# Kernel tuning notes

Measured on AMD Instinct MI355X. Metric: run time of the kernel, lower is better.

Reference implementation:

```python
import jax, jax.numpy as jnp
import numpy as np


def setup_inputs() -> dict:
    key = jax.random.key(0)
    k1, k2, k3 = jax.random.split(key, 3)
    B, S, D = 128, 1024, 64
    return {
        "q": jax.random.normal(k1, (B, S, D), dtype=jnp.float32),
        "k": jax.random.normal(k2, (B, S, D), dtype=jnp.float32),
        "v": jax.random.normal(k3, (B, S, D), dtype=jnp.float32),
    }


def reference(q, k, v):
    # Faithful to the torch module: NO 1/sqrt(d) scaling.
    # Chunking over batch dim in the original is math-equivalent to full bmm.
    scores = jnp.einsum("bsd,btd->bst", q, k)  # [B, S, S]
    attn = jax.nn.softmax(scores, axis=-1)
    return jnp.einsum("bst,btd->bsd", attn, v)  # [B, S, D]
```

## Files before the change

kernel.cpp:

```cpp
#include <hip/hip_runtime.h>
#include <math.h>

namespace {

typedef _Float16 half8 __attribute__((ext_vector_type(8)));
typedef float floatx4 __attribute__((ext_vector_type(4)));

constexpr int kS   = 1024;
constexpr int kD   = 64;
constexpr int kPad = 72;
constexpr float kLog2e = 1.4426950408889634f;
constexpr float kThr   = 8.0f;

union H4 { _Float16 h[4]; uint2 u2; };

__device__ __forceinline__ float fast_exp2(float x) {
#if __has_builtin(__builtin_amdgcn_exp2f)
  return __builtin_amdgcn_exp2f(x);
#else
  return exp2f(x);
#endif
}

__device__ __forceinline__ float fast_rcp(float x) {
#if __has_builtin(__builtin_amdgcn_rcpf)
  return __builtin_amdgcn_rcpf(x);
#else
  return 1.0f / x;
#endif
}

__device__ __forceinline__ unsigned pk2(float a, float b) {
#if __has_builtin(__builtin_amdgcn_cvt_pkrtz)
  auto h = __builtin_amdgcn_cvt_pkrtz(a, b);
  return __builtin_bit_cast(unsigned, h);
#else
  H4 t; t.h[0] = (_Float16)a; t.h[1] = (_Float16)b;
  return t.u2.x;
#endif
}

__global__ __launch_bounds__(256, 2)
void fa_mfma_kernel(const float* __restrict__ qg, const float* __restrict__ kg,
                    const float* __restrict__ vg, float* __restrict__ og) {
  __shared__ __align__(16) _Float16 sK [2][64][kPad];
  __shared__ __align__(16) _Float16 sVt[2][64][kPad];
  __shared__ __align__(16) _Float16 sP [256][kPad];

  const int tid  = threadIdx.x;
  const int lane = tid & 63;
  const int w    = __builtin_amdgcn_readfirstlane(tid >> 6);
  const int quad = lane >> 4;
  const int r    = lane & 15;

  const int blk = blockIdx.x;
  const int b     = (blk & 7) + 8 * (blk >> 5);
  const int qbase = ((blk >> 3) & 3) * 256;

  const float* qb = qg + (size_t)b * kS * kD;
  const float* kb = kg + (size_t)b * kS * kD;
  const float* vb = vg + (size_t)b * kS * kD;
  float*       ob = og + (size_t)b * kS * kD;

  half8 fqh[4][2], fql[4][2];
#pragma unroll
  for (int ntq = 0; ntq < 4; ++ntq)
#pragma unroll
    for (int ks = 0; ks < 2; ++ks) {
      const float* src =
          qb + (size_t)(qbase + w * 64 + ntq * 16 + r) * kD + ks * 32 + quad * 8;
      float4 a = ((const float4*)src)[0];
      float4 c = ((const float4*)src)[1];
      float f[8] = {a.x, a.y, a.z, a.w, c.x, c.y, c.z, c.w};
#pragma unroll
      for (int j = 0; j < 8; ++j) {
        float x = f[j] * kLog2e;
        _Float16 h = (_Float16)x;
        fqh[ntq][ks][j] = h;
        fql[ntq][ks][j] = (_Float16)(x - (float)h);
      }
    }

  float m_i[4] = {-INFINITY, -INFINITY, -INFINITY, -INFINITY};
  float l_i[4] = {0.f, 0.f, 0.f, 0.f};
  floatx4 O[4][4];
#pragma unroll
  for (int a = 0; a < 4; ++a)
#pragma unroll
    for (int c = 0; c < 4; ++c) O[a][c] = floatx4{0.f, 0.f, 0.f, 0.f};

  const int krow = tid >> 2, kc0 = (tid & 3) * 16;
  const int vkey4 = (tid & 15) * 4;
  const int vd0   = (tid >> 4) * 4;
  float4 kbuf[4], vbuf[4];

  auto load_kv = [&](int kt) {
    const float4* ksrc = (const float4*)(kb + (size_t)(kt * 64 + krow) * kD + kc0);
#pragma unroll
    for (int g = 0; g < 4; ++g) kbuf[g] = ksrc[g];
#pragma unroll
    for (int kk = 0; kk < 4; ++kk)
      vbuf[kk] = *(const float4*)(vb + (size_t)(kt * 64 + vkey4 + kk) * kD + vd0);
  };
  auto stage = [&](int bi) {
#pragma unroll
    for (int g = 0; g < 4; ++g) {
      float t[4] = {kbuf[g].x, kbuf[g].y, kbuf[g].z, kbuf[g].w};
      H4 hk;
#pragma unroll
      for (int j = 0; j < 4; ++j) hk.h[j] = (_Float16)t[j];
      *(uint2*)&sK[bi][krow][kc0 + g * 4] = hk.u2;
    }
    float tv[4][4];
#pragma unroll
    for (int kk = 0; kk < 4; ++kk) {
      tv[kk][0] = vbuf[kk].x; tv[kk][1] = vbuf[kk].y;
      tv[kk][2] = vbuf[kk].z; tv[kk][3] = vbuf[kk].w;
    }
#pragma unroll
    for (int j = 0; j < 4; ++j) {
      H4 hv;
#pragma unroll
      for (int kk = 0; kk < 4; ++kk) hv.h[kk] = (_Float16)tv[kk][j];
      *(uint2*)&sVt[bi][vd0 + j][vkey4] = hv.u2;
    }
  };

  auto softmax2 = [&](floatx4 (&S)[2][4], int base) {
    float pmax[2];
#pragma unroll
    for (int g = 0; g < 2; ++g) {
      float a0 = fmaxf(fmaxf(S[g][0][0], S[g][0][1]), fmaxf(S[g][0][2], S[g][0][3]));
      float a1 = fmaxf(fmaxf(S[g][1][0], S[g][1][1]), fmaxf(S[g][1][2], S[g][1][3]));
      float a2 = fmaxf(fmaxf(S[g][2][0], S[g][2][1]), fmaxf(S[g][2][2], S[g][2][3]));
      float a3 = fmaxf(fmaxf(S[g][3][0], S[g][3][1]), fmaxf(S[g][3][2], S[g][3][3]));
      pmax[g] = fmaxf(fmaxf(a0, a1), fmaxf(a2, a3));
    }
    const unsigned long long need =
        __ballot(pmax[0] > m_i[base] + kThr || pmax[1] > m_i[base + 1] + kThr);
    if (need) {
      float alpha[2];
#pragma unroll
      for (int g = 0; g < 2; ++g) {
        float t = pmax[g];
        t = fmaxf(t, __shfl_xor(t, 16, 64));
        t = fmaxf(t, __shfl_xor(t, 32, 64));
        const float mn = fmaxf(m_i[base + g], t);
        alpha[g] = fast_exp2(m_i[base + g] - mn);
        m_i[base + g] = mn;
        l_i[base + g] *= alpha[g];
      }
#pragma unroll
      for (int g = 0; g < 2; ++g)
#pragma unroll
        for (int j = 0; j < 4; ++j) {
          const float a = __shfl(alpha[g], quad * 4 + j, 64);
#pragma unroll
          for (int nd = 0; nd < 4; ++nd) O[base + g][nd][j] *= a;
        }
    }
#pragma unroll
    for (int g = 0; g < 2; ++g) {
      float rs = 0.f;
#pragma unroll
      for (int mt = 0; mt < 4; ++mt) {
        float p0 = fast_exp2(S[g][mt][0] - m_i[base + g]);
        float p1 = fast_exp2(S[g][mt][1] - m_i[base + g]);
        float p2 = fast_exp2(S[g][mt][2] - m_i[base + g]);
        float p3 = fast_exp2(S[g][mt][3] - m_i[base + g]);
        rs += (p0 + p1) + (p2 + p3);
        uint2 u; u.x = pk2(p0, p1); u.y = pk2(p2, p3);
        *(uint2*)&sP[w * 64 + (base + g) * 16 + r][mt * 16 + quad * 4] = u;
      }
      l_i[base + g] += rs;
    }
  };

  load_kv(0);
  stage(0);
  load_kv(1);

  for (int kt = 0; kt < kS / 64; ++kt) {
    const int cur = kt & 1, nxt = cur ^ 1;
    __syncthreads();
    stage(nxt);
    load_kv((kt + 2) & 15);

    floatx4 S0[2][4];
    __builtin_amdgcn_s_setprio(1);
#pragma unroll
    for (int mt = 0; mt < 4; ++mt) {
      half8 fk0 = *(const half8*)&sK[cur][mt * 16 + r][quad * 8];
      half8 fk1 = *(const half8*)&sK[cur][mt * 16 + r][32 + quad * 8];
#pragma unroll
      for (int g = 0; g < 2; ++g) {
        floatx4 s = {0.f, 0.f, 0.f, 0.f};
        s = __builtin_amdgcn_mfma_f32_16x16x32_f16(fk0, fqh[g][0], s, 0, 0, 0);
        s = __builtin_amdgcn_mfma_f32_16x16x32_f16(fk1, fqh[g][1], s, 0, 0, 0);
        s = __builtin_amdgcn_mfma_f32_16x16x32_f16(fk0, fql[g][0], s, 0, 0, 0);
        s = __builtin_amdgcn_mfma_f32_16x16x32_f16(fk1, fql[g][1], s, 0, 0, 0);
        S0[g][mt] = s;
      }
    }
    __builtin_amdgcn_s_setprio(0);

    softmax2(S0, 0);

    floatx4 S1[2][4];
    __builtin_amdgcn_s_setprio(1);
#pragma unroll
    for (int mt = 0; mt < 4; ++mt) {
      half8 fk0 = *(const half8*)&sK[cur][mt * 16 + r][quad * 8];
      half8 fk1 = *(const half8*)&sK[cur][mt * 16 + r][32 + quad * 8];
#pragma unroll
      for (int g = 0; g < 2; ++g) {
        floatx4 s = {0.f, 0.f, 0.f, 0.f};
        s = __builtin_amdgcn_mfma_f32_16x16x32_f16(fk0, fqh[2 + g][0], s, 0, 0, 0);
        s = __builtin_amdgcn_mfma_f32_16x16x32_f16(fk1, fqh[2 + g][1], s, 0, 0, 0);
        s = __builtin_amdgcn_mfma_f32_16x16x32_f16(fk0, fql[2 + g][0], s, 0, 0, 0);
        s = __builtin_amdgcn_mfma_f32_16x16x32_f16(fk1, fql[2 + g][1], s, 0, 0, 0);
        S1[g][mt] = s;
      }
    }
    __builtin_amdgcn_s_setprio(0);

    __builtin_amdgcn_s_setprio(1);
#pragma unroll
    for (int ks = 0; ks < 2; ++ks) {
      half8 fp0 = *(const half8*)&sP[w * 64 + 0 * 16 + r][ks * 32 + quad * 8];
      half8 fp1 = *(const half8*)&sP[w * 64 + 1 * 16 + r][ks * 32 + quad * 8];
#pragma unroll
      for (int nd = 0; nd < 4; ++nd) {
        half8 fv = *(const half8*)&sVt[cur][nd * 16 + r][ks * 32 + quad * 8];
        O[0][nd] = __builtin_amdgcn_mfma_f32_16x16x32_f16(fp0, fv, O[0][nd], 0, 0, 0);
        O[1][nd] = __builtin_amdgcn_mfma_f32_16x16x32_f16(fp1, fv, O[1][nd], 0, 0, 0);
      }
    }
    __builtin_amdgcn_s_setprio(0);

    softmax2(S1, 2);

    __builtin_amdgcn_s_setprio(1);
#pragma unroll
    for (int ks = 0; ks < 2; ++ks) {
      half8 fp2 = *(const half8*)&sP[w * 64 + 2 * 16 + r][ks * 32 + quad * 8];
      half8 fp3 = *(const half8*)&sP[w * 64 + 3 * 16 + r][ks * 32 + quad * 8];
#pragma unroll
      for (int nd = 0; nd < 4; ++nd) {
        half8 fv = *(const half8*)&sVt[cur][nd * 16 + r][ks * 32 + quad * 8];
        O[2][nd] = __builtin_amdgcn_mfma_f32_16x16x32_f16(fp2, fv, O[2][nd], 0, 0, 0);
        O[3][nd] = __builtin_amdgcn_mfma_f32_16x16x32_f16(fp3, fv, O[3][nd], 0, 0, 0);
      }
    }
    __builtin_amdgcn_s_setprio(0);
  }

#pragma unroll
  for (int mtq = 0; mtq < 4; ++mtq) {
    float t = l_i[mtq];
    t += __shfl_xor(t, 16, 64);
    t += __shfl_xor(t, 32, 64);
#pragma unroll
    for (int j = 0; j < 4; ++j) {
      const float lrow = __shfl(t, quad * 4 + j, 64);
      const float linv = fast_rcp(lrow);
      float* dst =
          ob + (size_t)(qbase + w * 64 + mtq * 16 + quad * 4 + j) * kD + r;
#pragma unroll
      for (int nd = 0; nd < 4; ++nd) dst[nd * 16] = O[mtq][nd][j] * linv;
    }
  }
}

}

extern "C" void kernel_launch(void* const* d_in, const int* in_sizes, int n_in,
                              void* d_out, int out_size, void* d_ws, size_t ws_size,
                              hipStream_t stream) {
  const float* q = (const float*)d_in[0];
  const float* k = (const float*)d_in[1];
  const float* v = (const float*)d_in[2];
  float* out = (float*)d_out;

  fa_mfma_kernel<<<dim3(512), 256, 0, stream>>>(q, k, v, out);
}
```

Baseline: 191.5 us.

## Load K fragments directly from global into registers, drop K LDS staging

K tiles are now read straight from global memory into per-lane MFMA fragments (converted to fp16 in registers) instead of being staged through shared memory. The next K tile is prefetched after the second softmax. The two PV MFMA blocks are merged into a single pass after both softmaxes. The row-max reduction now runs before the ballot, and the row-sum reduction runs every tile rather than once at the end. This removes LDS traffic and the K staging step, but adds redundant global reads of K (each wave loads the full tile), more registers, and extra shuffles on every tile.

```diff
diff --git a/kernel.cpp b/kernel.cpp
--- a/kernel.cpp
+++ b/kernel.cpp
@@ -30,20 +30,9 @@
 #endif
 }
 
-__device__ __forceinline__ unsigned pk2(float a, float b) {
-#if __has_builtin(__builtin_amdgcn_cvt_pkrtz)
-  auto h = __builtin_amdgcn_cvt_pkrtz(a, b);
-  return __builtin_bit_cast(unsigned, h);
-#else
-  H4 t; t.h[0] = (_Float16)a; t.h[1] = (_Float16)b;
-  return t.u2.x;
-#endif
-}
-
 __global__ __launch_bounds__(256, 2)
 void fa_mfma_kernel(const float* __restrict__ qg, const float* __restrict__ kg,
                     const float* __restrict__ vg, float* __restrict__ og) {
-  __shared__ __align__(16) _Float16 sK [2][64][kPad];
   __shared__ __align__(16) _Float16 sVt[2][64][kPad];
   __shared__ __align__(16) _Float16 sP [256][kPad];
 
@@ -89,28 +78,34 @@
 #pragma unroll
     for (int c = 0; c < 4; ++c) O[a][c] = floatx4{0.f, 0.f, 0.f, 0.f};
 
-  const int krow = tid >> 2, kc0 = (tid & 3) * 16;
+  half8 fk[4][2];
+  auto load_k = [&](int kt) {
+#pragma unroll
+    for (int mt = 0; mt < 4; ++mt)
+#pragma unroll
+      for (int ks = 0; ks < 2; ++ks) {
+        const float* s =
+            kb + (size_t)(kt * 64 + mt * 16 + r) * kD + ks * 32 + quad * 8;
+        float4 a = ((const float4*)s)[0];
+        float4 c = ((const float4*)s)[1];
+        half8 h;
+        h[0] = (_Float16)a.x; h[1] = (_Float16)a.y;
+        h[2] = (_Float16)a.z; h[3] = (_Float16)a.w;
+        h[4] = (_Float16)c.x; h[5] = (_Float16)c.y;
+        h[6] = (_Float16)c.z; h[7] = (_Float16)c.w;
+        fk[mt][ks] = h;
+      }
+  };
+
   const int vkey4 = (tid & 15) * 4;
   const int vd0   = (tid >> 4) * 4;
-  float4 kbuf[4], vbuf[4];
-
-  auto load_kv = [&](int kt) {
-    const float4* ksrc = (const float4*)(kb + (size_t)(kt * 64 + krow) * kD + kc0);
-#pragma unroll
-    for (int g = 0; g < 4; ++g) kbuf[g] = ksrc[g];
+  float4 vbuf[4];
+  auto load_v = [&](int kt) {
 #pragma unroll
     for (int kk = 0; kk < 4; ++kk)
       vbuf[kk] = *(const float4*)(vb + (size_t)(kt * 64 + vkey4 + kk) * kD + vd0);
   };
-  auto stage = [&](int bi) {
-#pragma unroll
-    for (int g = 0; g < 4; ++g) {
-      float t[4] = {kbuf[g].x, kbuf[g].y, kbuf[g].z, kbuf[g].w};
-      H4 hk;
-#pragma unroll
-      for (int j = 0; j < 4; ++j) hk.h[j] = (_Float16)t[j];
-      *(uint2*)&sK[bi][krow][kc0 + g * 4] = hk.u2;
-    }
+  auto stage_v = [&](int bi) {
     float tv[4][4];
 #pragma unroll
     for (int kk = 0; kk < 4; ++kk) {
@@ -127,25 +122,25 @@
   };
 
   auto softmax2 = [&](floatx4 (&S)[2][4], int base) {
-    float pmax[2];
+    float tm[2];
 #pragma unroll
     for (int g = 0; g < 2; ++g) {
       float a0 = fmaxf(fmaxf(S[g][0][0], S[g][0][1]), fmaxf(S[g][0][2], S[g][0][3]));
       float a1 = fmaxf(fmaxf(S[g][1][0], S[g][1][1]), fmaxf(S[g][1][2], S[g][1][3]));
       float a2 = fmaxf(fmaxf(S[g][2][0], S[g][2][1]), fmaxf(S[g][2][2], S[g][2][3]));
       float a3 = fmaxf(fmaxf(S[g][3][0], S[g][3][1]), fmaxf(S[g][3][2], S[g][3][3]));
-      pmax[g] = fmaxf(fmaxf(a0, a1), fmaxf(a2, a3));
+      float t = fmaxf(fmaxf(a0, a1), fmaxf(a2, a3));
+      t = fmaxf(t, __shfl_xor(t, 16, 64));
+      t = fmaxf(t, __shfl_xor(t, 32, 64));
+      tm[g] = t;
     }
     const unsigned long long need =
-        __ballot(pmax[0] > m_i[base] + kThr || pmax[1] > m_i[base + 1] + kThr);
+        __ballot(tm[0] > m_i[base] + kThr || tm[1] > m_i[base + 1] + kThr);
     if (need) {
       float alpha[2];
 #pragma unroll
       for (int g = 0; g < 2; ++g) {
-        float t = pmax[g];
-        t = fmaxf(t, __shfl_xor(t, 16, 64));
-        t = fmaxf(t, __shfl_xor(t, 32, 64));
-        const float mn = fmaxf(m_i[base + g], t);
+        const float mn = fmaxf(m_i[base + g], tm[g]);
         alpha[g] = fast_exp2(m_i[base + g] - mn);
         m_i[base + g] = mn;
         l_i[base + g] *= alpha[g];
@@ -164,44 +159,45 @@
       float rs = 0.f;
 #pragma unroll
       for (int mt = 0; mt < 4; ++mt) {
-        float p0 = fast_exp2(S[g][mt][0] - m_i[base + g]);
-        float p1 = fast_exp2(S[g][mt][1] - m_i[base + g]);
-        float p2 = fast_exp2(S[g][mt][2] - m_i[base + g]);
-        float p3 = fast_exp2(S[g][mt][3] - m_i[base + g]);
-        rs += (p0 + p1) + (p2 + p3);
-        uint2 u; u.x = pk2(p0, p1); u.y = pk2(p2, p3);
-        *(uint2*)&sP[w * 64 + (base + g) * 16 + r][mt * 16 + quad * 4] = u;
-      }
+        H4 hp;
+#pragma unroll
+        for (int j = 0; j < 4; ++j) {
+          float pj = fast_exp2(S[g][mt][j] - m_i[base + g]);
+          rs += pj;
+          hp.h[j] = (_Float16)pj;
+        }
+        *(uint2*)&sP[w * 64 + (base + g) * 16 + r][mt * 16 + quad * 4] = hp.u2;
+      }
+      rs += __shfl_xor(rs, 16, 64);
+      rs += __shfl_xor(rs, 32, 64);
       l_i[base + g] += rs;
     }
   };
 
-  load_kv(0);
-  stage(0);
-  load_kv(1);
+  load_k(0);
+  load_v(0);
+  stage_v(0);
+  load_v(1);
 
   for (int kt = 0; kt < kS / 64; ++kt) {
     const int cur = kt & 1, nxt = cur ^ 1;
     __syncthreads();
-    stage(nxt);
-    load_kv((kt + 2) & 15);
+    stage_v(nxt);
+    load_v((kt + 2) & 15);
 
     floatx4 S0[2][4];
     __builtin_amdgcn_s_setprio(1);
 #pragma unroll
-    for (int mt = 0; mt < 4; ++mt) {
-      half8 fk0 = *(const half8*)&sK[cur][mt * 16 + r][quad * 8];
-      half8 fk1 = *(const half8*)&sK[cur][mt * 16 + r][32 + quad * 8];
+    for (int mt = 0; mt < 4; ++mt)
 #pragma unroll
       for (int g = 0; g < 2; ++g) {
         floatx4 s = {0.f, 0.f, 0.f, 0.f};
-        s = __builtin_amdgcn_mfma_f32_16x16x32_f16(fk0, fqh[g][0], s, 0, 0, 0);
-        s = __builtin_amdgcn_mfma_f32_16x16x32_f16(fk1, fqh[g][1], s, 0, 0, 0);
-        s = __builtin_amdgcn_mfma_f32_16x16x32_f16(fk0, fql[g][0], s, 0, 0, 0);
-        s = __builtin_amdgcn_mfma_f32_16x16x32_f16(fk1, fql[g][1], s, 0, 0, 0);
+        s = __builtin_amdgcn_mfma_f32_16x16x32_f16(fk[mt][0], fqh[g][0], s, 0, 0, 0);
+        s = __builtin_amdgcn_mfma_f32_16x16x32_f16(fk[mt][1], fqh[g][1], s, 0, 0, 0);
+        s = __builtin_amdgcn_mfma_f32_16x16x32_f16(fk[mt][0], fql[g][0], s, 0, 0, 0);
+        s = __builtin_amdgcn_mfma_f32_16x16x32_f16(fk[mt][1], fql[g][1], s, 0, 0, 0);
         S0[g][mt] = s;
       }
-    }
     __builtin_amdgcn_s_setprio(0);
 
     softmax2(S0, 0);
@@ -209,45 +205,34 @@
     floatx4 S1[2][4];
     __builtin_amdgcn_s_setprio(1);
 #pragma unroll
-    for (int mt = 0; mt < 4; ++mt) {
-      half8 fk0 = *(const half8*)&sK[cur][mt * 16 + r][quad * 8];
-      half8 fk1 = *(const half8*)&sK[cur][mt * 16 + r][32 + quad * 8];
+    for (int mt = 0; mt < 4; ++mt)
 #pragma unroll
       for (int g = 0; g < 2; ++g) {
         floatx4 s = {0.f, 0.f, 0.f, 0.f};
-        s = __builtin_amdgcn_mfma_f32_16x16x32_f16(fk0, fqh[2 + g][0], s, 0, 0, 0);
-        s = __builtin_amdgcn_mfma_f32_16x16x32_f16(fk1, fqh[2 + g][1], s, 0, 0, 0);
-        s = __builtin_amdgcn_mfma_f32_16x16x32_f16(fk0, fql[2 + g][0], s, 0, 0, 0);
-        s = __builtin_amdgcn_mfma_f32_16x16x32_f16(fk1, fql[2 + g][1], s, 0, 0, 0);
+        s = __builtin_amdgcn_mfma_f32_16x16x32_f16(fk[mt][0], fqh[2 + g][0], s, 0, 0, 0);
+        s = __builtin_amdgcn_mfma_f32_16x16x32_f16(fk[mt][1], fqh[2 + g][1], s, 0, 0, 0);
+        s = __builtin_amdgcn_mfma_f32_16x16x32_f16(fk[mt][0], fql[2 + g][0], s, 0, 0, 0);
+        s = __builtin_amdgcn_mfma_f32_16x16x32_f16(fk[mt][1], fql[2 + g][1], s, 0, 0, 0);
         S1[g][mt] = s;
       }
-    }
     __builtin_amdgcn_s_setprio(0);
+
+    softmax2(S1, 2);
+
+    load_k((kt + 1) & 15);
 
     __builtin_amdgcn_s_setprio(1);
 #pragma unroll
     for (int ks = 0; ks < 2; ++ks) {
       half8 fp0 = *(const half8*)&sP[w * 64 + 0 * 16 + r][ks * 32 + quad * 8];
       half8 fp1 = *(const half8*)&sP[w * 64 + 1 * 16 + r][ks * 32 + quad * 8];
+      half8 fp2 = *(const half8*)&sP[w * 64 + 2 * 16 + r][ks * 32 + quad * 8];
+      half8 fp3 = *(const half8*)&sP[w * 64 + 3 * 16 + r][ks * 32 + quad * 8];
 #pragma unroll
       for (int nd = 0; nd < 4; ++nd) {
         half8 fv = *(const half8*)&sVt[cur][nd * 16 + r][ks * 32 + quad * 8];
         O[0][nd] = __builtin_amdgcn_mfma_f32_16x16x32_f16(fp0, fv, O[0][nd], 0, 0, 0);
         O[1][nd] = __builtin_amdgcn_mfma_f32_16x16x32_f16(fp1, fv, O[1][nd], 0, 0, 0);
-      }
-    }
-    __builtin_amdgcn_s_setprio(0);
-
-    softmax2(S1, 2);
-
-    __builtin_amdgcn_s_setprio(1);
-#pragma unroll
-    for (int ks = 0; ks < 2; ++ks) {
-      half8 fp2 = *(const half8*)&sP[w * 64 + 2 * 16 + r][ks * 32 + quad * 8];
-      half8 fp3 = *(const half8*)&sP[w * 64 + 3 * 16 + r][ks * 32 + quad * 8];
-#pragma unroll
-      for (int nd = 0; nd < 4; ++nd) {
-        half8 fv = *(const half8*)&sVt[cur][nd * 16 + r][ks * 32 + quad * 8];
         O[2][nd] = __builtin_amdgcn_mfma_f32_16x16x32_f16(fp2, fv, O[2][nd], 0, 0, 0);
         O[3][nd] = __builtin_amdgcn_mfma_f32_16x16x32_f16(fp3, fv, O[3][nd], 0, 0, 0);
       }
@@ -256,20 +241,16 @@
   }
 
 #pragma unroll
-  for (int mtq = 0; mtq < 4; ++mtq) {
-    float t = l_i[mtq];
-    t += __shfl_xor(t, 16, 64);
-    t += __shfl_xor(t, 32, 64);
+  for (int mtq = 0; mtq < 4; ++mtq)
 #pragma unroll
     for (int j = 0; j < 4; ++j) {
-      const float lrow = __shfl(t, quad * 4 + j, 64);
+      const float lrow = __shfl(l_i[mtq], quad * 4 + j, 64);
       const float linv = fast_rcp(lrow);
       float* dst =
           ob + (size_t)(qbase + w * 64 + mtq * 16 + quad * 4 + j) * kD + r;
 #pragma unroll
       for (int nd = 0; nd < 4; ++nd) dst[nd * 16] = O[mtq][nd][j] * linv;
     }
-  }
 }
 
 }
```

Result: slower. 224.2 us (+17.1%).
